# Kernel optimization log

Measured on AMD Instinct MI355X. Metric: run time of the kernel, lower is better.

Reference implementation:

```python
import jax, jax.numpy as jnp
import numpy as np

N = 100000        # nodes
E = 3200000       # directed edges (before self-loops)
IN_CH = 500
HID = 256
HEADS = 8
C = HID // HEADS  # 32 per-head channels
OUT_CH = 40
NEG_SLOPE = 0.2   # PyG GATConv default


def _gat_conv(x, W, a_src, a_dst, b, src, dst):
    """PyG-style GATConv (concat=True, self-loops already in src/dst, eval mode)."""
    n = x.shape[0]
    h = (x @ W).reshape(n, HEADS, C)                      # [N, H, C]
    # per-node attention logits
    e_src = jnp.einsum('nhc,hc->nh', h, a_src)            # source contribution
    e_dst = jnp.einsum('nhc,hc->nh', h, a_dst)            # target contribution
    e = jax.nn.leaky_relu(e_src[src] + e_dst[dst], NEG_SLOPE)  # [E, H]
    # segment softmax over incoming edges of each destination node
    m = jax.ops.segment_max(e, dst, num_segments=n)       # [N, H]
    e = jnp.exp(e - m[dst])
    s = jax.ops.segment_sum(e, dst, num_segments=n)       # [N, H]
    alpha = e / (s[dst] + 1e-16)                          # [E, H]
    msg = h[src] * alpha[:, :, None]                      # [E, H, C]
    out = jax.ops.segment_sum(msg, dst, num_segments=n)   # [N, H, C]
    return out.reshape(n, HEADS * C) + b


def setup_inputs() -> dict:
    key = jax.random.key(0)
    ks = jax.random.split(key, 20)
    x = jax.random.normal(ks[0], (N, IN_CH), jnp.float32)
    edge_index = jax.random.randint(ks[1], (2, E), 0, N, dtype=jnp.int64)

    def glorot(k, shape):
        fan = shape[0] + shape[-1]
        return jax.random.normal(k, shape, jnp.float32) * jnp.sqrt(2.0 / fan)

    inp = {"x": x, "edge_index": edge_index}
    in_dims = [IN_CH, HID, HID]
    for i in range(3):
        inp[f"W{i}"] = glorot(ks[2 + 4 * i], (in_dims[i], HID))
        inp[f"a_src{i}"] = glorot(ks[3 + 4 * i], (HEADS, C))
        inp[f"a_dst{i}"] = glorot(ks[4 + 4 * i], (HEADS, C))
        inp[f"b{i}"] = jnp.zeros((HID,), jnp.float32)
    inp["Wf"] = glorot(ks[15], (HID, OUT_CH))
    inp["bf"] = jnp.zeros((OUT_CH,), jnp.float32)
    return inp


def reference(x, edge_index, W0, a_src0, a_dst0, b0, W1, a_src1, a_dst1, b1,
              W2, a_src2, a_dst2, b2, Wf, bf):
    # add self loops (PyG GATConv default)
    loop = jnp.arange(N, dtype=edge_index.dtype)
    src = jnp.concatenate([edge_index[0], loop])
    dst = jnp.concatenate([edge_index[1], loop])

    h0 = jax.nn.elu(_gat_conv(x, W0, a_src0, a_dst0, b0, src, dst))
    h1 = jax.nn.elu(_gat_conv(h0, W1, a_src1, a_dst1, b1, src, dst))
    h2 = _gat_conv(h1, W2, a_src2, a_dst2, b2, src, dst)  # last conv: no activation
    # JumpingKnowledge 'max': elementwise max over layer outputs
    jk = jnp.maximum(jnp.maximum(h0, h1), h2)
    logits = jk @ Wf + bf
    return jax.nn.log_softmax(logits, axis=1)
```

## Files before the change

### kernel.cpp

```cpp
#include <hip/hip_runtime.h>
#include <hip/hip_bf16.h>
#include <math.h>

#define HID 256
#define HEADS 8
#define KP0 512
#define EPB 16384
#define NBMAX 1024
#define FKG 16

typedef __attribute__((ext_vector_type(8))) short short8;
typedef __attribute__((ext_vector_type(4))) float floatx4;
typedef __attribute__((ext_vector_type(4))) unsigned uintx4;

__device__ __forceinline__ void gl_lds16(const void* g, void* l) {
  __builtin_amdgcn_global_load_lds(
      (const __attribute__((address_space(1))) void*)g,
      (__attribute__((address_space(3))) void*)l, 16, 0, 0);
}

__device__ __forceinline__ float blo(unsigned u) { return __uint_as_float(u << 16); }
__device__ __forceinline__ float bhi(unsigned u) { return __uint_as_float(u & 0xffff0000u); }

__device__ __forceinline__ void acc8(float* acc, uintx4 g, float w) {
  acc[0] += w * blo(g[0]); acc[1] += w * bhi(g[0]);
  acc[2] += w * blo(g[1]); acc[3] += w * bhi(g[1]);
  acc[4] += w * blo(g[2]); acc[5] += w * bhi(g[2]);
  acc[6] += w * blo(g[3]); acc[7] += w * bhi(g[3]);
}


__global__ __launch_bounds__(256) void edge_hist_kernel(const int* __restrict__ ei,
    int* __restrict__ F, int E, int Etot, int NB, int NBLK) {
  __shared__ int hist[NBMAX];
  int blk = blockIdx.x, t = threadIdx.x;
  for (int i = t; i < NBMAX; i += 256) hist[i] = 0;
  __syncthreads();
  int base = blk * EPB;
  int lim = min(EPB, Etot - base);
  for (int i = t; i < lim; i += 256) {
    int idx = base + i;
    int d = (idx < E) ? ei[E + idx] : (idx - E);
    atomicAdd(&hist[d >> 7], 1);
  }
  __syncthreads();
  for (int b = t; b < NB; b += 256) F[b * NBLK + blk] = hist[b];
}

__global__ __launch_bounds__(256) void scan_part_kernel(const int* __restrict__ F,
    int* __restrict__ bsum, int L) {
  __shared__ int ws[4];
  int blk = blockIdx.x, t = threadIdx.x;
  int base = blk * 1024 + t * 4;
  int s = 0;
  if (base + 3 < L) {
    int4 v = *(const int4*)(F + base);
    s = v.x + v.y + v.z + v.w;
  } else {
    for (int i = 0; i < 4; ++i) if (base + i < L) s += F[base + i];
  }
#pragma unroll
  for (int off = 1; off < 64; off <<= 1) s += __shfl_xor(s, off);
  if ((t & 63) == 0) ws[t >> 6] = s;
  __syncthreads();
  if (t == 0) bsum[blk] = ws[0] + ws[1] + ws[2] + ws[3];
}

__global__ __launch_bounds__(256) void scan_bsum_kernel(const int* __restrict__ bsum,
    int* __restrict__ bb, int* __restrict__ S, int NBS, int L) {
  __shared__ int ps[256];
  int t = threadIdx.x;
  int v = (t < NBS) ? bsum[t] : 0;
  ps[t] = v;
  __syncthreads();
  for (int off = 1; off < 256; off <<= 1) {
    int add = (t >= off) ? ps[t - off] : 0;
    __syncthreads();
    ps[t] += add;
    __syncthreads();
  }
  if (t < NBS) bb[t] = (t == 0) ? 0 : ps[t - 1];
  if (t == 255) S[L] = ps[255];
}

__global__ __launch_bounds__(256) void scan_apply_kernel(const int* __restrict__ F,
    const int* __restrict__ bb, int* __restrict__ S, int L) {
  __shared__ int ps[256];
  int blk = blockIdx.x, t = threadIdx.x;
  int base = blk * 1024 + t * 4;
  int v0 = 0, v1 = 0, v2 = 0, v3 = 0;
  if (base + 3 < L) {
    int4 w = *(const int4*)(F + base);
    v0 = w.x; v1 = w.y; v2 = w.z; v3 = w.w;
  } else {
    if (base + 0 < L) v0 = F[base + 0];
    if (base + 1 < L) v1 = F[base + 1];
    if (base + 2 < L) v2 = F[base + 2];
    if (base + 3 < L) v3 = F[base + 3];
  }
  ps[t] = v0 + v1 + v2 + v3;
  __syncthreads();
  for (int off = 1; off < 256; off <<= 1) {
    int add = (t >= off) ? ps[t - off] : 0;
    __syncthreads();
    ps[t] += add;
    __syncthreads();
  }
  int run = bb[blk] + ((t == 0) ? 0 : ps[t - 1]);
  if (base + 0 < L) S[base + 0] = run; run += v0;
  if (base + 1 < L) S[base + 1] = run; run += v1;
  if (base + 2 < L) S[base + 2] = run; run += v2;
  if (base + 3 < L) S[base + 3] = run;
}

__global__ __launch_bounds__(256) void edge_scatter_kernel(const int* __restrict__ ei,
    const int* __restrict__ S, unsigned* __restrict__ stag, int E, int Etot,
    int NB, int NBLK) {
  __shared__ int cur[NBMAX];
  int blk = blockIdx.x, t = threadIdx.x;
  for (int b = t; b < NB; b += 256) cur[b] = S[b * NBLK + blk];
  __syncthreads();
  int base = blk * EPB;
  int lim = min(EPB, Etot - base);
  for (int i = t; i < lim; i += 256) {
    int idx = base + i;
    int s, d;
    if (idx < E) { s = ei[idx]; d = ei[E + idx]; }
    else { s = idx - E; d = s; }
    int pos = atomicAdd(&cur[d >> 7], 1);
    stag[pos] = ((unsigned)(d & 127) << 17) | (unsigned)s;
  }
}

__global__ __launch_bounds__(256) void bucket_build_kernel(const unsigned* __restrict__ stag,
    const int* __restrict__ S, int NBLK,
    int* __restrict__ rowptr, int* __restrict__ csr_src, int N) {
  __shared__ int deg[128], pfx[128], cur[128];
  int b = blockIdx.x;
  int t = threadIdx.x;
  int gbase = S[(size_t)b * NBLK];
  int gend = S[(size_t)(b + 1) * NBLK];
  int cnt = gend - gbase;
  int node0 = b << 7;
  int nn = min(128, N - node0);
  if (t < 128) deg[t] = 0;
  __syncthreads();
  const unsigned* sb = stag + gbase;
  for (int i = t; i < cnt; i += 256) atomicAdd(&deg[sb[i] >> 17], 1);
  __syncthreads();
  if (t == 0) {
    int run = 0;
#pragma unroll 8
    for (int i = 0; i < 128; ++i) { pfx[i] = run; run += deg[i]; }
  }
  __syncthreads();
  if (t < 128) cur[t] = pfx[t];
  if (t < nn) rowptr[node0 + t] = gbase + pfx[t];
  if (b == (int)gridDim.x - 1 && t == 0) rowptr[N] = gbase + cnt;
  __syncthreads();
  for (int i = t; i < cnt; i += 256) {
    unsigned v = sb[i];
    int dl = v >> 17;
    int pos = gbase + atomicAdd(&cur[dl], 1);
    csr_src[pos] = (int)(v & 0x1ffff);
  }
}


__global__ __launch_bounds__(256) void conv_x_kernel(const float* __restrict__ x,
    __hip_bfloat16* __restrict__ xb, int M, int K) {
  long idx = (long)blockIdx.x * 256 + threadIdx.x;
  if (idx >= (long)M * (KP0 / 8)) return;
  int n = (int)(idx >> 6);
  int k0 = ((int)idx & 63) * 8;
  const float* xr = x + (size_t)n * K;
  float4 a = {0.f, 0.f, 0.f, 0.f}, b = {0.f, 0.f, 0.f, 0.f};
  if (k0 + 3 < K) a = *(const float4*)(xr + k0);
  else {
    if (k0 + 0 < K) a.x = xr[k0 + 0];
    if (k0 + 1 < K) a.y = xr[k0 + 1];
    if (k0 + 2 < K) a.z = xr[k0 + 2];
    if (k0 + 3 < K) a.w = xr[k0 + 3];
  }
  if (k0 + 7 < K) b = *(const float4*)(xr + k0 + 4);
  else {
    if (k0 + 4 < K) b.x = xr[k0 + 4];
    if (k0 + 5 < K) b.y = xr[k0 + 5];
    if (k0 + 6 < K) b.z = xr[k0 + 6];
    if (k0 + 7 < K) b.w = xr[k0 + 7];
  }
  union { short8 v; __hip_bfloat16 h[8]; } o;
  o.h[0] = __float2bfloat16(a.x); o.h[1] = __float2bfloat16(a.y);
  o.h[2] = __float2bfloat16(a.z); o.h[3] = __float2bfloat16(a.w);
  o.h[4] = __float2bfloat16(b.x); o.h[5] = __float2bfloat16(b.y);
  o.h[6] = __float2bfloat16(b.z); o.h[7] = __float2bfloat16(b.w);
  *(short8*)(xb + (size_t)n * KP0 + k0) = o.v;
}

__global__ __launch_bounds__(256) void convT_w_kernel(const float* __restrict__ W,
    __hip_bfloat16* __restrict__ Wt, int K, int Kp) {
  int idx = blockIdx.x * 256 + threadIdx.x;
  if (idx >= 256 * Kp) return;
  int n = idx / Kp, k = idx - n * Kp;
  Wt[idx] = __float2bfloat16((k < K) ? W[(size_t)k * 256 + n] : 0.f);
}


__global__ __launch_bounds__(256) void gemm_mfma(const __hip_bfloat16* __restrict__ A,
    const __hip_bfloat16* __restrict__ Bt, __hip_bfloat16* __restrict__ C,
    int M, int Kp) {
  __shared__ __align__(16) __hip_bfloat16 As[128][32];
  __shared__ __align__(16) __hip_bfloat16 Bs[128][32];
  int tid = threadIdx.x;
  int wave = tid >> 6, lane = tid & 63;
  int quad = lane >> 4, mr = lane & 15;
  int row0 = blockIdx.x * 128, col0 = blockIdx.y * 128;
  int wm = (wave & 1) * 64, wn = (wave >> 1) * 64;
  floatx4 acc[4][4] = {};

  int srow = (lane >> 2);
  int kslot = lane & 3;
  int kc = (kslot ^ (srow & 3)) * 8;

  for (int k0 = 0; k0 < Kp; k0 += 32) {
#pragma unroll
    for (int j = 0; j < 2; ++j) {
      int r = wave * 32 + j * 16 + srow;
      gl_lds16(A + (size_t)(row0 + r) * Kp + k0 + kc, &As[wave * 32 + j * 16][0]);
      gl_lds16(Bt + (size_t)(col0 + r) * Kp + k0 + kc, &Bs[wave * 32 + j * 16][0]);
    }
    __syncthreads();
    short8 af[4], bfr[4];
#pragma unroll
    for (int r = 0; r < 4; ++r) {
      int row = wm + r * 16 + mr;
      af[r] = *(const short8*)&As[row][(quad ^ (row & 3)) * 8];
      int col = wn + r * 16 + mr;
      bfr[r] = *(const short8*)&Bs[col][(quad ^ (col & 3)) * 8];
    }
#pragma unroll
    for (int r = 0; r < 4; ++r)
#pragma unroll
      for (int c = 0; c < 4; ++c)
        acc[r][c] = __builtin_amdgcn_mfma_f32_16x16x32_bf16(af[r], bfr[c], acc[r][c], 0, 0, 0);
    __syncthreads();
  }
#pragma unroll
  for (int r = 0; r < 4; ++r) {
#pragma unroll
    for (int c = 0; c < 4; ++c) {
#pragma unroll
      for (int i = 0; i < 4; ++i) {
        int row = row0 + wm + r * 16 + quad * 4 + i;
        int col = wn + c * 16 + mr + col0;
        if (row < M) C[(size_t)row * HID + col] = __float2bfloat16(acc[r][c][i]);
      }
    }
  }
}


__global__ __launch_bounds__(256) void node_logits_kernel(const __hip_bfloat16* __restrict__ H,
    const float* __restrict__ a_src, const float* __restrict__ a_dst,
    float* __restrict__ en_src, float* __restrict__ en_dst, int N) {
  int idx = blockIdx.x * 256 + threadIdx.x;
  if (idx >= N * HEADS) return;
  int n = idx >> 3, h = idx & 7;
  const uint4* Hp = (const uint4*)(H + (size_t)n * HID + h * 32);
  const float* S = a_src + h * 32;
  const float* D = a_dst + h * 32;
  float es = 0.f, ed = 0.f;
#pragma unroll
  for (int j = 0; j < 4; ++j) {
    uint4 u = Hp[j];
    unsigned w[4] = {u.x, u.y, u.z, u.w};
#pragma unroll
    for (int p = 0; p < 4; ++p) {
      float lo = blo(w[p]);
      float hi = bhi(w[p]);
      int c = j * 8 + p * 2;
      es += lo * S[c] + hi * S[c + 1];
      ed += lo * D[c] + hi * D[c + 1];
    }
  }
  en_src[idx] = es;
  en_dst[idx] = ed;
}


__global__ __launch_bounds__(256) void gat_agg_kernel(const __hip_bfloat16* __restrict__ H,
    const float* __restrict__ en_src, const float* __restrict__ en_dst,
    const int* __restrict__ rowptr, const int* __restrict__ csr_src,
    const float* __restrict__ bias, __hip_bfloat16* __restrict__ hb,
    int apply_elu, int N) {
  int wave = threadIdx.x >> 6;
  int lane = threadIdx.x & 63;
  int n = blockIdx.x * 4 + wave;
  if (n >= N) return;
  int h = lane >> 3;
  int slot = lane & 7;
  int beg = rowptr[n], end = rowptr[n + 1];
  float ed = en_dst[n * HEADS + h];

  float m = -1e30f, s = 0.f;
  for (int e = beg + slot; e < end; e += 8) {
    int src = csr_src[e];
    float v = en_src[src * HEADS + h] + ed;
    v = (v > 0.f) ? v : 0.2f * v;
    float mn = fmaxf(m, v);
    s = s * __expf(m - mn) + __expf(v - mn);
    m = mn;
  }
#pragma unroll
  for (int off = 1; off < 8; off <<= 1) {
    float mo = __shfl_xor(m, off);
    float so = __shfl_xor(s, off);
    float mn = fmaxf(m, mo);
    s = s * __expf(m - mn) + so * __expf(mo - mn);
    m = mn;
  }
  float rs = 1.f / (s + 1e-16f);

  int eo = lane >> 5;
  int cl = lane & 31;
  int hh = cl >> 2;
  float m2 = __shfl(m, hh * 8);
  float rs2 = __shfl(rs, hh * 8);
  float ed2 = __shfl(ed, hh * 8);

  float acc[8] = {0.f, 0.f, 0.f, 0.f, 0.f, 0.f, 0.f, 0.f};
  const __hip_bfloat16* Hc = H + cl * 8;
  for (int cs = beg; cs < end; cs += 64) {
    int cnt = min(64, end - cs);
    int myidx = csr_src[cs + ((lane < cnt) ? lane : (cnt - 1))];
    int i = 0;
    for (; i + 8 <= cnt; i += 8) {
      int s0 = __shfl(myidx, i + eo);
      int s1 = __shfl(myidx, i + 2 + eo);
      int s2 = __shfl(myidx, i + 4 + eo);
      int s3 = __shfl(myidx, i + 6 + eo);
      uintx4 g0 = *(const uintx4*)(Hc + (size_t)s0 * HID);
      uintx4 g1 = *(const uintx4*)(Hc + (size_t)s1 * HID);
      uintx4 g2 = *(const uintx4*)(Hc + (size_t)s2 * HID);
      uintx4 g3 = *(const uintx4*)(Hc + (size_t)s3 * HID);
      float v0 = en_src[s0 * HEADS + hh] + ed2;
      float v1 = en_src[s1 * HEADS + hh] + ed2;
      float v2 = en_src[s2 * HEADS + hh] + ed2;
      float v3 = en_src[s3 * HEADS + hh] + ed2;
      v0 = (v0 > 0.f) ? v0 : 0.2f * v0;
      v1 = (v1 > 0.f) ? v1 : 0.2f * v1;
      v2 = (v2 > 0.f) ? v2 : 0.2f * v2;
      v3 = (v3 > 0.f) ? v3 : 0.2f * v3;
      float w0 = __expf(v0 - m2) * rs2;
      float w1 = __expf(v1 - m2) * rs2;
      float w2 = __expf(v2 - m2) * rs2;
      float w3 = __expf(v3 - m2) * rs2;
      acc8(acc, g0, w0);
      acc8(acc, g1, w1);
      acc8(acc, g2, w2);
      acc8(acc, g3, w3);
    }
    for (; i + 4 <= cnt; i += 4) {
      int sa = __shfl(myidx, i + eo);
      int sb = __shfl(myidx, i + 2 + eo);
      uintx4 ga = *(const uintx4*)(Hc + (size_t)sa * HID);
      uintx4 gb = *(const uintx4*)(Hc + (size_t)sb * HID);
      float va = en_src[sa * HEADS + hh] + ed2;
      float vb = en_src[sb * HEADS + hh] + ed2;
      va = (va > 0.f) ? va : 0.2f * va;
      vb = (vb > 0.f) ? vb : 0.2f * vb;
      float wa = __expf(va - m2) * rs2;
      float wb = __expf(vb - m2) * rs2;
      acc8(acc, ga, wa);
      acc8(acc, gb, wb);
    }
    for (; i < cnt; i += 2) {
      int j = i + eo;
      int jj = (j < cnt) ? j : (cnt - 1);
      int sa = __shfl(myidx, jj);
      uintx4 ga = *(const uintx4*)(Hc + (size_t)sa * HID);
      float va = en_src[sa * HEADS + hh] + ed2;
      va = (va > 0.f) ? va : 0.2f * va;
      float wa = (j < cnt) ? __expf(va - m2) * rs2 : 0.f;
      acc8(acc, ga, wa);
    }
  }
#pragma unroll
  for (int i = 0; i < 8; ++i) acc[i] += __shfl_xor(acc[i], 32);

  if (eo == 0) {
    const float4* bp = (const float4*)(bias + cl * 8);
    float4 b0 = bp[0], b1 = bp[1];
    float o[8];
    o[0] = acc[0] + b0.x; o[1] = acc[1] + b0.y;
    o[2] = acc[2] + b0.z; o[3] = acc[3] + b0.w;
    o[4] = acc[4] + b1.x; o[5] = acc[5] + b1.y;
    o[6] = acc[6] + b1.z; o[7] = acc[7] + b1.w;
    if (apply_elu) {
#pragma unroll
      for (int i = 0; i < 8; ++i) o[i] = (o[i] > 0.f) ? o[i] : expm1f(o[i]);
    }
    union { __hip_bfloat16 hh8[8]; uintx4 u; } pk;
#pragma unroll
    for (int i = 0; i < 8; ++i) pk.hh8[i] = __float2bfloat16(o[i]);
    __builtin_nontemporal_store(pk.u, (uintx4*)(hb + (size_t)n * HID + cl * 8));
  }
}


__global__ __launch_bounds__(256) void final_kernel(const __hip_bfloat16* __restrict__ hb0,
    const __hip_bfloat16* __restrict__ hb1, const __hip_bfloat16* __restrict__ hb2,
    const float* __restrict__ Wf, const float* __restrict__ bf,
    float* __restrict__ out, int N) {
  __shared__ float Wfs[HID * 40];
  __shared__ float jks[4][HID];
  int tid = threadIdx.x;
  for (int i = tid; i < HID * 40; i += 256) Wfs[i] = Wf[i];
  int sub = tid >> 6, lane = tid & 63;
  int nbase = blockIdx.x * 4 * FKG;
  __syncthreads();
  for (int g = 0; g < FKG; ++g) {
    int n = nbase + g * 4 + sub;
    if (n < N) {
      uint2 a = *(const uint2*)(hb0 + (size_t)n * HID + lane * 4);
      uint2 b = *(const uint2*)(hb1 + (size_t)n * HID + lane * 4);
      uint2 c = *(const uint2*)(hb2 + (size_t)n * HID + lane * 4);
      float4 r;
      r.x = fmaxf(fmaxf(blo(a.x), blo(b.x)), blo(c.x));
      r.y = fmaxf(fmaxf(bhi(a.x), bhi(b.x)), bhi(c.x));
      r.z = fmaxf(fmaxf(blo(a.y), blo(b.y)), blo(c.y));
      r.w = fmaxf(fmaxf(bhi(a.y), bhi(b.y)), bhi(c.y));
      *(float4*)&jks[sub][lane * 4] = r;
    }
    __syncthreads();
    float logit = -INFINITY;
    if (lane < 40 && n < N) {
      float accv = bf[lane];
#pragma unroll 8
      for (int k = 0; k < HID; ++k) accv += jks[sub][k] * Wfs[k * 40 + lane];
      logit = accv;
    }
    float mx = logit;
#pragma unroll
    for (int off = 32; off > 0; off >>= 1) mx = fmaxf(mx, __shfl_down(mx, off));
    mx = __shfl(mx, 0);
    float ex = (lane < 40 && n < N) ? __expf(logit - mx) : 0.f;
    float sm = ex;
#pragma unroll
    for (int off = 32; off > 0; off >>= 1) sm += __shfl_down(sm, off);
    sm = __shfl(sm, 0);
    if (lane < 40 && n < N) out[(size_t)n * 40 + lane] = logit - mx - __logf(sm);
    __syncthreads();
  }
}


extern "C" void kernel_launch(void* const* d_in, const int* in_sizes, int n_in,
                              void* d_out, int out_size, void* d_ws, size_t ws_size,
                              hipStream_t stream) {
  (void)n_in; (void)out_size; (void)ws_size;
  const float* x   = (const float*)d_in[0];
  const int*   ei  = (const int*)d_in[1];
  const float* W0  = (const float*)d_in[2];
  const float* as0 = (const float*)d_in[3];
  const float* ad0 = (const float*)d_in[4];
  const float* b0  = (const float*)d_in[5];
  const float* W1  = (const float*)d_in[6];
  const float* as1 = (const float*)d_in[7];
  const float* ad1 = (const float*)d_in[8];
  const float* b1  = (const float*)d_in[9];
  const float* W2  = (const float*)d_in[10];
  const float* as2 = (const float*)d_in[11];
  const float* ad2 = (const float*)d_in[12];
  const float* b2  = (const float*)d_in[13];
  const float* Wf  = (const float*)d_in[14];
  const float* bf  = (const float*)d_in[15];
  float* out = (float*)d_out;

  const int E = in_sizes[1] / 2;
  const int IN_CH = in_sizes[2] / HID;
  const int N = in_sizes[0] / IN_CH;
  const int Etot = E + N;
  const int Mp = ((N + 127) / 128) * 128;
  const int NB = (N + 127) >> 7;
  const int NBLK = (Etot + EPB - 1) / EPB;
  const int L = NB * NBLK;
  const int NBS = (L + 1023) / 1024;
  const size_t NM = (size_t)N * HID;
  const size_t MpM = (size_t)Mp * HID;

  __hip_bfloat16* xb  = (__hip_bfloat16*)d_ws;
  __hip_bfloat16* Htb = xb + (size_t)Mp * KP0;
  __hip_bfloat16* hb0 = Htb + NM;
  __hip_bfloat16* hb1 = hb0 + MpM;
  __hip_bfloat16* hb2 = hb1 + MpM;
  __hip_bfloat16* Wt0 = hb2 + MpM;
  __hip_bfloat16* Wt1 = Wt0 + 256 * KP0;
  __hip_bfloat16* Wt2 = Wt1 + 256 * 256;
  float* fbase = (float*)(Wt2 + 256 * 256);
  float* en_s = fbase;
  float* en_d = en_s + (size_t)N * HEADS;
  int* rowptr  = (int*)(en_d + (size_t)N * HEADS);
  int* csr_src = rowptr + (((size_t)N + 1 + 3) & ~(size_t)3);
  int* F       = csr_src + (((size_t)Etot + 3) & ~(size_t)3);
  int* S       = F + (((size_t)L + 3) & ~(size_t)3);
  int* bsum    = S + (((size_t)L + 1 + 3) & ~(size_t)3);
  int* bb      = bsum + 256;
  unsigned* stag = (unsigned*)(bb + 256);

  edge_hist_kernel<<<NBLK, 256, 0, stream>>>(ei, F, E, Etot, NB, NBLK);
  scan_part_kernel<<<NBS, 256, 0, stream>>>(F, bsum, L);
  scan_bsum_kernel<<<1, 256, 0, stream>>>(bsum, bb, S, NBS, L);
  scan_apply_kernel<<<NBS, 256, 0, stream>>>(F, bb, S, L);
  edge_scatter_kernel<<<NBLK, 256, 0, stream>>>(ei, S, stag, E, Etot, NB, NBLK);
  bucket_build_kernel<<<NB, 256, 0, stream>>>(stag, S, NBLK, rowptr, csr_src, N);

  conv_x_kernel<<<((size_t)N * (KP0 / 8) + 255) / 256, 256, 0, stream>>>(x, xb, N, IN_CH);
  convT_w_kernel<<<(256 * KP0 + 255) / 256, 256, 0, stream>>>(W0, Wt0, IN_CH, KP0);
  convT_w_kernel<<<(256 * 256 + 255) / 256, 256, 0, stream>>>(W1, Wt1, HID, HID);
  convT_w_kernel<<<(256 * 256 + 255) / 256, 256, 0, stream>>>(W2, Wt2, HID, HID);

  dim3 ggrid(Mp / 128, 2);
  int lblocks = (N * HEADS + 255) / 256;
  int ablocks = (N + 3) / 4;
  int fblocks = (N + 4 * FKG - 1) / (4 * FKG);

  gemm_mfma<<<ggrid, 256, 0, stream>>>(xb, Wt0, Htb, N, KP0);
  node_logits_kernel<<<lblocks, 256, 0, stream>>>(Htb, as0, ad0, en_s, en_d, N);
  gat_agg_kernel<<<ablocks, 256, 0, stream>>>(Htb, en_s, en_d, rowptr, csr_src, b0, hb0, 1, N);
  gemm_mfma<<<ggrid, 256, 0, stream>>>(hb0, Wt1, Htb, N, HID);
  node_logits_kernel<<<lblocks, 256, 0, stream>>>(Htb, as1, ad1, en_s, en_d, N);
  gat_agg_kernel<<<ablocks, 256, 0, stream>>>(Htb, en_s, en_d, rowptr, csr_src, b1, hb1, 1, N);
  gemm_mfma<<<ggrid, 256, 0, stream>>>(hb1, Wt2, Htb, N, HID);
  node_logits_kernel<<<lblocks, 256, 0, stream>>>(Htb, as2, ad2, en_s, en_d, N);
  gat_agg_kernel<<<ablocks, 256, 0, stream>>>(Htb, en_s, en_d, rowptr, csr_src, b2, hb2, 0, N);

  final_kernel<<<fblocks, 256, 0, stream>>>(hb0, hb1, hb2, Wf, bf, out, N);
}
```

Measured before the change: 1.729 ms.

## Fuse fp32-to-bf16 input conversion and attention logits into full-width GEMM

The first-layer GEMM now reads fp32 x directly, converts it to bf16 and stores it into LDS, which removes the separate conversion kernel and its padded bf16 buffer. The node_logits kernel is gone: the per-head source and destination attention logits are computed from the fp32 accumulators in the GEMM epilogue with cross-lane shuffles. Each GEMM block now covers all 256 output columns with 512 threads, so A tiles are loaded once instead of twice. The cost is a register-staged A load in the first layer instead of direct-to-LDS loads, a heavier epilogue, and logits computed from unrounded fp32 values rather than the stored bf16 features.

```diff
diff --git a/kernel.cpp b/kernel.cpp
--- a/kernel.cpp
+++ b/kernel.cpp
@@ -167,36 +167,6 @@
 }
 
 
-__global__ __launch_bounds__(256) void conv_x_kernel(const float* __restrict__ x,
-    __hip_bfloat16* __restrict__ xb, int M, int K) {
-  long idx = (long)blockIdx.x * 256 + threadIdx.x;
-  if (idx >= (long)M * (KP0 / 8)) return;
-  int n = (int)(idx >> 6);
-  int k0 = ((int)idx & 63) * 8;
-  const float* xr = x + (size_t)n * K;
-  float4 a = {0.f, 0.f, 0.f, 0.f}, b = {0.f, 0.f, 0.f, 0.f};
-  if (k0 + 3 < K) a = *(const float4*)(xr + k0);
-  else {
-    if (k0 + 0 < K) a.x = xr[k0 + 0];
-    if (k0 + 1 < K) a.y = xr[k0 + 1];
-    if (k0 + 2 < K) a.z = xr[k0 + 2];
-    if (k0 + 3 < K) a.w = xr[k0 + 3];
-  }
-  if (k0 + 7 < K) b = *(const float4*)(xr + k0 + 4);
-  else {
-    if (k0 + 4 < K) b.x = xr[k0 + 4];
-    if (k0 + 5 < K) b.y = xr[k0 + 5];
-    if (k0 + 6 < K) b.z = xr[k0 + 6];
-    if (k0 + 7 < K) b.w = xr[k0 + 7];
-  }
-  union { short8 v; __hip_bfloat16 h[8]; } o;
-  o.h[0] = __float2bfloat16(a.x); o.h[1] = __float2bfloat16(a.y);
-  o.h[2] = __float2bfloat16(a.z); o.h[3] = __float2bfloat16(a.w);
-  o.h[4] = __float2bfloat16(b.x); o.h[5] = __float2bfloat16(b.y);
-  o.h[6] = __float2bfloat16(b.z); o.h[7] = __float2bfloat16(b.w);
-  *(short8*)(xb + (size_t)n * KP0 + k0) = o.v;
-}
-
 __global__ __launch_bounds__(256) void convT_w_kernel(const float* __restrict__ W,
     __hip_bfloat16* __restrict__ Wt, int K, int Kp) {
   int idx = blockIdx.x * 256 + threadIdx.x;
@@ -206,29 +176,81 @@
 }
 
 
-__global__ __launch_bounds__(256) void gemm_mfma(const __hip_bfloat16* __restrict__ A,
+__device__ __forceinline__ void gemm_epilogue(floatx4 (&acc)[4][4],
+    __hip_bfloat16* __restrict__ C, float* __restrict__ en_s, float* __restrict__ en_d,
+    const float* __restrict__ a_src, const float* __restrict__ a_dst,
+    int row0, int wm, int wn, int quad, int mr, int M) {
+#pragma unroll
+  for (int r = 0; r < 4; ++r) {
+#pragma unroll
+    for (int c = 0; c < 4; ++c) {
+#pragma unroll
+      for (int i = 0; i < 4; ++i) {
+        int row = row0 + wm + r * 16 + quad * 4 + i;
+        int col = wn + c * 16 + mr;
+        if (row < M) C[(size_t)row * HID + col] = __float2bfloat16(acc[r][c][i]);
+      }
+    }
+  }
+  float as_c[4], ad_c[4];
+#pragma unroll
+  for (int c = 0; c < 4; ++c) {
+    int col = wn + c * 16 + mr;
+    as_c[c] = a_src[col];
+    ad_c[c] = a_dst[col];
+  }
+  int h0 = wn >> 5;
+#pragma unroll
+  for (int r = 0; r < 4; ++r) {
+#pragma unroll
+    for (int i = 0; i < 4; ++i) {
+      float e0 = acc[r][0][i] * as_c[0] + acc[r][1][i] * as_c[1];
+      float e1 = acc[r][2][i] * as_c[2] + acc[r][3][i] * as_c[3];
+      float d0 = acc[r][0][i] * ad_c[0] + acc[r][1][i] * ad_c[1];
+      float d1 = acc[r][2][i] * ad_c[2] + acc[r][3][i] * ad_c[3];
+#pragma unroll
+      for (int off = 1; off < 16; off <<= 1) {
+        e0 += __shfl_xor(e0, off);
+        e1 += __shfl_xor(e1, off);
+        d0 += __shfl_xor(d0, off);
+        d1 += __shfl_xor(d1, off);
+      }
+      if (mr == 0) {
+        int row = row0 + wm + r * 16 + quad * 4 + i;
+        if (row < M) {
+          en_s[row * HEADS + h0] = e0;
+          en_s[row * HEADS + h0 + 1] = e1;
+          en_d[row * HEADS + h0] = d0;
+          en_d[row * HEADS + h0 + 1] = d1;
+        }
+      }
+    }
+  }
+}
+
+
+__global__ __launch_bounds__(512) void gemm_bf16(const __hip_bfloat16* __restrict__ A,
     const __hip_bfloat16* __restrict__ Bt, __hip_bfloat16* __restrict__ C,
+    float* __restrict__ en_s, float* __restrict__ en_d,
+    const float* __restrict__ a_src, const float* __restrict__ a_dst,
     int M, int Kp) {
   __shared__ __align__(16) __hip_bfloat16 As[128][32];
-  __shared__ __align__(16) __hip_bfloat16 Bs[128][32];
+  __shared__ __align__(16) __hip_bfloat16 Bs[256][32];
   int tid = threadIdx.x;
   int wave = tid >> 6, lane = tid & 63;
   int quad = lane >> 4, mr = lane & 15;
-  int row0 = blockIdx.x * 128, col0 = blockIdx.y * 128;
+  int row0 = blockIdx.x * 128;
   int wm = (wave & 1) * 64, wn = (wave >> 1) * 64;
   floatx4 acc[4][4] = {};
-
-  int srow = (lane >> 2);
+  int srow = lane >> 2;
   int kslot = lane & 3;
   int kc = (kslot ^ (srow & 3)) * 8;
 
   for (int k0 = 0; k0 < Kp; k0 += 32) {
-#pragma unroll
-    for (int j = 0; j < 2; ++j) {
-      int r = wave * 32 + j * 16 + srow;
-      gl_lds16(A + (size_t)(row0 + r) * Kp + k0 + kc, &As[wave * 32 + j * 16][0]);
-      gl_lds16(Bt + (size_t)(col0 + r) * Kp + k0 + kc, &Bs[wave * 32 + j * 16][0]);
-    }
+    gl_lds16(A + (size_t)(row0 + wave * 16 + srow) * Kp + k0 + kc, &As[wave * 16][0]);
+#pragma unroll
+    for (int j = 0; j < 2; ++j)
+      gl_lds16(Bt + (size_t)(wave * 32 + j * 16 + srow) * Kp + k0 + kc, &Bs[wave * 32 + j * 16][0]);
     __syncthreads();
     short8 af[4], bfr[4];
 #pragma unroll
@@ -245,46 +267,68 @@
         acc[r][c] = __builtin_amdgcn_mfma_f32_16x16x32_bf16(af[r], bfr[c], acc[r][c], 0, 0, 0);
     __syncthreads();
   }
-#pragma unroll
-  for (int r = 0; r < 4; ++r) {
-#pragma unroll
-    for (int c = 0; c < 4; ++c) {
-#pragma unroll
-      for (int i = 0; i < 4; ++i) {
-        int row = row0 + wm + r * 16 + quad * 4 + i;
-        int col = wn + c * 16 + mr + col0;
-        if (row < M) C[(size_t)row * HID + col] = __float2bfloat16(acc[r][c][i]);
+  gemm_epilogue(acc, C, en_s, en_d, a_src, a_dst, row0, wm, wn, quad, mr, M);
+}
+
+
+__global__ __launch_bounds__(512) void gemm_f32a(const float* __restrict__ X,
+    const __hip_bfloat16* __restrict__ Bt, __hip_bfloat16* __restrict__ C,
+    float* __restrict__ en_s, float* __restrict__ en_d,
+    const float* __restrict__ a_src, const float* __restrict__ a_dst,
+    int M, int K, int Kp) {
+  __shared__ __align__(16) __hip_bfloat16 As[128][32];
+  __shared__ __align__(16) __hip_bfloat16 Bs[256][32];
+  int tid = threadIdx.x;
+  int wave = tid >> 6, lane = tid & 63;
+  int quad = lane >> 4, mr = lane & 15;
+  int row0 = blockIdx.x * 128;
+  int wm = (wave & 1) * 64, wn = (wave >> 1) * 64;
+  floatx4 acc[4][4] = {};
+  int srow = lane >> 2;
+  int kslot = lane & 3;
+  int kc = (kslot ^ (srow & 3)) * 8;
+
+  for (int k0 = 0; k0 < Kp; k0 += 32) {
+    {
+      int row = row0 + wave * 16 + srow;
+      int kg = k0 + kc;
+      float v[8];
+      if (row < M && kg + 7 < K) {
+        const float* xp = X + (size_t)row * K + kg;
+        float4 a = *(const float4*)xp;
+        float4 b = *(const float4*)(xp + 4);
+        v[0] = a.x; v[1] = a.y; v[2] = a.z; v[3] = a.w;
+        v[4] = b.x; v[5] = b.y; v[6] = b.z; v[7] = b.w;
+      } else {
+#pragma unroll
+        for (int j = 0; j < 8; ++j)
+          v[j] = (row < M && kg + j < K) ? X[(size_t)row * K + kg + j] : 0.f;
       }
-    }
-  }
-}
-
-
-__global__ __launch_bounds__(256) void node_logits_kernel(const __hip_bfloat16* __restrict__ H,
-    const float* __restrict__ a_src, const float* __restrict__ a_dst,
-    float* __restrict__ en_src, float* __restrict__ en_dst, int N) {
-  int idx = blockIdx.x * 256 + threadIdx.x;
-  if (idx >= N * HEADS) return;
-  int n = idx >> 3, h = idx & 7;
-  const uint4* Hp = (const uint4*)(H + (size_t)n * HID + h * 32);
-  const float* S = a_src + h * 32;
-  const float* D = a_dst + h * 32;
-  float es = 0.f, ed = 0.f;
-#pragma unroll
-  for (int j = 0; j < 4; ++j) {
-    uint4 u = Hp[j];
-    unsigned w[4] = {u.x, u.y, u.z, u.w};
-#pragma unroll
-    for (int p = 0; p < 4; ++p) {
-      float lo = blo(w[p]);
-      float hi = bhi(w[p]);
-      int c = j * 8 + p * 2;
-      es += lo * S[c] + hi * S[c + 1];
-      ed += lo * D[c] + hi * D[c + 1];
-    }
-  }
-  en_src[idx] = es;
-  en_dst[idx] = ed;
+      union { short8 s; __hip_bfloat16 h[8]; } pk;
+#pragma unroll
+      for (int j = 0; j < 8; ++j) pk.h[j] = __float2bfloat16(v[j]);
+      *(short8*)&As[wave * 16 + srow][kslot * 8] = pk.s;
+    }
+#pragma unroll
+    for (int j = 0; j < 2; ++j)
+      gl_lds16(Bt + (size_t)(wave * 32 + j * 16 + srow) * Kp + k0 + kc, &Bs[wave * 32 + j * 16][0]);
+    __syncthreads();
+    short8 af[4], bfr[4];
+#pragma unroll
+    for (int r = 0; r < 4; ++r) {
+      int row = wm + r * 16 + mr;
+      af[r] = *(const short8*)&As[row][(quad ^ (row & 3)) * 8];
+      int col = wn + r * 16 + mr;
+      bfr[r] = *(const short8*)&Bs[col][(quad ^ (col & 3)) * 8];
+    }
+#pragma unroll
+    for (int r = 0; r < 4; ++r)
+#pragma unroll
+      for (int c = 0; c < 4; ++c)
+        acc[r][c] = __builtin_amdgcn_mfma_f32_16x16x32_bf16(af[r], bfr[c], acc[r][c], 0, 0, 0);
+    __syncthreads();
+  }
+  gemm_epilogue(acc, C, en_s, en_d, a_src, a_dst, row0, wm, wn, quad, mr, M);
 }
 
 
@@ -489,8 +533,7 @@
   const size_t NM = (size_t)N * HID;
   const size_t MpM = (size_t)Mp * HID;
 
-  __hip_bfloat16* xb  = (__hip_bfloat16*)d_ws;
-  __hip_bfloat16* Htb = xb + (size_t)Mp * KP0;
+  __hip_bfloat16* Htb = (__hip_bfloat16*)d_ws;
   __hip_bfloat16* hb0 = Htb + NM;
   __hip_bfloat16* hb1 = hb0 + MpM;
   __hip_bfloat16* hb2 = hb1 + MpM;
@@ -515,24 +558,19 @@
   edge_scatter_kernel<<<NBLK, 256, 0, stream>>>(ei, S, stag, E, Etot, NB, NBLK);
   bucket_build_kernel<<<NB, 256, 0, stream>>>(stag, S, NBLK, rowptr, csr_src, N);
 
-  conv_x_kernel<<<((size_t)N * (KP0 / 8) + 255) / 256, 256, 0, stream>>>(x, xb, N, IN_CH);
   convT_w_kernel<<<(256 * KP0 + 255) / 256, 256, 0, stream>>>(W0, Wt0, IN_CH, KP0);
   convT_w_kernel<<<(256 * 256 + 255) / 256, 256, 0, stream>>>(W1, Wt1, HID, HID);
   convT_w_kernel<<<(256 * 256 + 255) / 256, 256, 0, stream>>>(W2, Wt2, HID, HID);
 
-  dim3 ggrid(Mp / 128, 2);
-  int lblocks = (N * HEADS + 255) / 256;
+  int gblocks = Mp / 128;
   int ablocks = (N + 3) / 4;
   int fblocks = (N + 4 * FKG - 1) / (4 * FKG);
 
-  gemm_mfma<<<ggrid, 256, 0, stream>>>(xb, Wt0, Htb, N, KP0);
-  node_logits_kernel<<<lblocks, 256, 0, stream>>>(Htb, as0, ad0, en_s, en_d, N);
+  gemm_f32a<<<gblocks, 512, 0, stream>>>(x, Wt0, Htb, en_s, en_d, as0, ad0, N, IN_CH, KP0);
   gat_agg_kernel<<<ablocks, 256, 0, stream>>>(Htb, en_s, en_d, rowptr, csr_src, b0, hb0, 1, N);
-  gemm_mfma<<<ggrid, 256, 0, stream>>>(hb0, Wt1, Htb, N, HID);
-  node_logits_kernel<<<lblocks, 256, 0, stream>>>(Htb, as1, ad1, en_s, en_d, N);
+  gemm_bf16<<<gblocks, 512, 0, stream>>>(hb0, Wt1, Htb, en_s, en_d, as1, ad1, N, HID);
   gat_agg_kernel<<<ablocks, 256, 0, stream>>>(Htb, en_s, en_d, rowptr, csr_src, b1, hb1, 1, N);
-  gemm_mfma<<<ggrid, 256, 0, stream>>>(hb1, Wt2, Htb, N, HID);
-  node_logits_kernel<<<lblocks, 256, 0, stream>>>(Htb, as2, ad2, en_s, en_d, N);
+  gemm_bf16<<<gblocks, 512, 0, stream>>>(hb1, Wt2, Htb, en_s, en_d, as2, ad2, N, HID);
   gat_agg_kernel<<<ablocks, 256, 0, stream>>>(Htb, en_s, en_d, rowptr, csr_src, b2, hb2, 0, N);
 
   final_kernel<<<fblocks, 256, 0, stream>>>(hb0, hb1, hb2, Wf, bf, out, N);
```

New measurement: 1.692 ms. 2.1% less time.
